# Kernel optimization log

Hardware: AMD Instinct MI355X
Metric: run time of the kernel (lower is better)

The kernel has to match this reference:

```python
import jax, jax.numpy as jnp
import numpy as np
from jax import lax

B, S, D, H, O = 128, 256, 128, 512, 25
TEMP = 0.1


def _init(key, shape, scale):
    return jax.random.uniform(key, shape, jnp.float32, -scale, scale)


def setup_inputs() -> dict:
    key = jax.random.key(0)
    ks = jax.random.split(key, 24)
    sH = 1.0 / np.sqrt(H)
    s2H = 1.0 / np.sqrt(2 * H)
    sD = 1.0 / np.sqrt(D)
    inp = {
        "x": jax.random.normal(ks[0], (B, S, D), jnp.float32),
        "noise_u": jnp.clip(jax.random.uniform(ks[1], (S, B, 1), jnp.float32), 1e-6, 1 - 1e-6),
        # layer_cin: Linear(D, H)
        "w_cin": _init(ks[2], (D, H), sD), "b_cin": _init(ks[3], (H,), sD),
        # layer_c MLP: 2H->2H (x3, ReLU) -> 1
        "w1": _init(ks[4], (2 * H, 2 * H), s2H), "b1": _init(ks[5], (2 * H,), s2H),
        "w2": _init(ks[6], (2 * H, 2 * H), s2H), "b2": _init(ks[7], (2 * H,), s2H),
        "w3": _init(ks[8], (2 * H, 2 * H), s2H), "b3": _init(ks[9], (2 * H,), s2H),
        "w4": _init(ks[10], (2 * H, 1), s2H), "b4": _init(ks[11], (1,), s2H),
        # GRUCell(H, H): gates ordered (r, z, n)
        "w_ih": _init(ks[12], (H, 3 * H), sH), "b_ih": _init(ks[13], (3 * H,), sH),
        "w_hh": _init(ks[14], (H, 3 * H), sH), "b_hh": _init(ks[15], (3 * H,), sH),
        # output Linear(H, O)
        "w_out": _init(ks[16], (H, O), sH), "b_out": _init(ks[17], (O,), sH),
    }
    return inp


def _gru_cell(x, h, w_ih, b_ih, w_hh, b_hh):
    gx = x @ w_ih + b_ih  # [B, 3H]
    gh = h @ w_hh + b_hh
    xr, xz, xn = jnp.split(gx, 3, axis=-1)
    hr, hz, hn = jnp.split(gh, 3, axis=-1)
    r = jax.nn.sigmoid(xr + hr)
    z = jax.nn.sigmoid(xz + hz)
    n = jnp.tanh(xn + r * hn)
    return (1.0 - z) * n + z * h


def reference(x, noise_u, w_cin, b_cin, w1, b1, w2, b2, w3, b3, w4, b4,
              w_ih, b_ih, w_hh, b_hh, w_out, b_out):
    xs = jnp.transpose(x, (1, 0, 2))  # [S, B, D]

    def step(carry, inp):
        c, h, n = carry
        x_t, u = inp
        c_in = jnp.tanh(x_t @ w_cin + b_cin)  # [B, H]
        com = jnp.concatenate([c, c_in], axis=1)  # [B, 2H]
        z = jax.nn.relu(com @ w1 + b1)
        z = jax.nn.relu(z @ w2 + b2)
        z = jax.nn.relu(z @ w3 + b3)
        alpha_logit = z @ w4 + b4  # [B, 1]
        # RelaxedBernoulli(temp=0.1).sample(): sigmoid((logits + logistic noise)/T), detached
        logistic = jnp.log(u) - jnp.log1p(-u)
        alpha = lax.stop_gradient(jax.nn.sigmoid((alpha_logit + logistic) / TEMP))
        h_gru = _gru_cell(c, h, w_ih, b_ih, w_hh, b_hh)
        h_new = h * (1.0 - alpha) + alpha * h_gru
        new_n = n * (1.0 - alpha) + 1.0
        c_new = (c * n * (1.0 - alpha) + c_in) / new_n
        return (c_new, h_new, new_n), None

    c0 = jnp.zeros((B, H), x.dtype)
    h0 = jnp.zeros((B, H), x.dtype)
    n0 = jnp.zeros((B, 1), x.dtype)
    (c, h, n), _ = lax.scan(step, (c0, h0, n0), (xs, noise_u))
    h = _gru_cell(c, h, w_ih, b_ih, w_hh, b_hh)  # final post-loop GRU step
    return h @ w_out + b_out
```

## Files before the change

### kernel.cpp

```cpp
#include <hip/hip_runtime.h>
#include <math.h>

#define SLEN 256
#define BSZ  128
#define DIN  128
#define HSZ  512
#define HH2  1024
#define GG3  1536
#define OSZ  25
#define SPIN_LIMIT (1 << 22)

typedef _Float16 h8 __attribute__((ext_vector_type(8)));
typedef _Float16 h4v __attribute__((ext_vector_type(4)));
typedef float    f4 __attribute__((ext_vector_type(4)));

struct P_t {
  const float *x, *noise, *b_cin, *b1, *b2, *b3, *w4, *b4, *b_ih, *b_hh, *w_out, *b_out;
  _Float16 *WT1, *WT2, *WT3, *WTih, *WThh, *WTcin;
  _Float16 *FW1T, *FW1B, *FW2, *FW3, *FWih, *FWhh;
  _Float16 *CIN, *Z1, *Z2, *HGRU16;
  float *LOGI, *C1, *D1, *CIH, *G;
  float *A1, *AIH, *AHH, *HF, *HGRUF, *NF, *PART;
  int *CNT;
  float *out;
};

__device__ __forceinline__ f4 mfma16(h8 a, h8 b, f4 c) {
  return __builtin_amdgcn_mfma_f32_16x16x32_f16(a, b, c, 0, 0, 0);
}

__global__ __launch_bounds__(256) void transpose_cvt(const float* __restrict__ src,
    _Float16* __restrict__ dst, int K, int N) {
  __shared__ float tl[32][33];
  int nt = N >> 5;
  int bx = blockIdx.x % nt, by = blockIdx.x / nt;
  int n0 = bx << 5, k0 = by << 5;
  int tx = threadIdx.x & 31, ty = threadIdx.x >> 5;
#pragma unroll
  for (int i = 0; i < 4; ++i) {
    int r = ty + (i << 3);
    tl[r][tx] = src[(size_t)(k0 + r) * N + n0 + tx];
  }
  __syncthreads();
#pragma unroll
  for (int i = 0; i < 4; ++i) {
    int r = ty + (i << 3);
    dst[(size_t)(n0 + r) * K + k0 + tx] = (_Float16)tl[tx][r];
  }
}

__global__ __launch_bounds__(512) void fragpack2(const _Float16* __restrict__ src,
    _Float16* __restrict__ dst, int srcK, int kOff, int K) {
  int ct = blockIdx.x;
  int chunks = (K / 32) * 64;
  for (int idx = threadIdx.x; idx < chunks; idx += 512) {
    int i = idx >> 6, lane = idx & 63;
    int mlw = lane & 15, qw = lane >> 4;
    *(h8*)(dst + ((size_t)ct * (K / 32) + i) * 512 + (size_t)lane * 8) =
        *(const h8*)(src + ((size_t)ct * 16 + mlw) * srcK + kOff + i * 32 + qw * 8);
  }
}

__global__ __launch_bounds__(256) void cin_kernel(P_t P) {
  int tid = blockIdx.x * blockDim.x + threadIdx.x;
  if (tid < SLEN * BSZ) {
    float u = P.noise[tid];
    P.LOGI[tid] = logf(u) - log1pf(-u);
  }
  int gw = tid >> 6, lane = tid & 63;
  int nw = (gridDim.x * blockDim.x) >> 6;
  int ml = lane & 15, q = lane >> 4;
  const int MT = (SLEN * BSZ) / 16;
  for (int tt = gw; tt < MT * 8; tt += nw) {
    int mt = tt & (MT - 1), nt = tt / MT;
    int m0 = mt * 16, n0 = nt * 64;
    int m = m0 + ml, b = m & 127, s = m >> 7;
    const float* ap = P.x + ((size_t)b * SLEN + s) * DIN + q * 8;
    const _Float16* bp = P.WTcin + (size_t)(n0 + ml) * DIN + q * 8;
    f4 a0 = {0,0,0,0}, a1 = a0, a2 = a0, a3 = a0;
#pragma unroll
    for (int k = 0; k < DIN; k += 32) {
      f4 lo = *(const f4*)(ap + k);
      f4 hi = *(const f4*)(ap + k + 4);
      h8 av;
      av[0] = (_Float16)lo[0]; av[1] = (_Float16)lo[1];
      av[2] = (_Float16)lo[2]; av[3] = (_Float16)lo[3];
      av[4] = (_Float16)hi[0]; av[5] = (_Float16)hi[1];
      av[6] = (_Float16)hi[2]; av[7] = (_Float16)hi[3];
      a0 = mfma16(av, *(const h8*)(bp + k),            a0);
      a1 = mfma16(av, *(const h8*)(bp + 16*DIN + k),   a1);
      a2 = mfma16(av, *(const h8*)(bp + 32*DIN + k),   a2);
      a3 = mfma16(av, *(const h8*)(bp + 48*DIN + k),   a3);
    }
#pragma unroll
    for (int r = 0; r < 4; ++r) {
      int row = m0 + q * 4 + r;
      int c0 = n0 + ml;
      P.CIN[(size_t)row * HSZ + c0     ] = (_Float16)tanhf(a0[r] + P.b_cin[c0]);
      P.CIN[(size_t)row * HSZ + c0 + 16] = (_Float16)tanhf(a1[r] + P.b_cin[c0 + 16]);
      P.CIN[(size_t)row * HSZ + c0 + 32] = (_Float16)tanhf(a2[r] + P.b_cin[c0 + 32]);
      P.CIN[(size_t)row * HSZ + c0 + 48] = (_Float16)tanhf(a3[r] + P.b_cin[c0 + 48]);
    }
  }
}

__global__ __launch_bounds__(256) void init_kernel(P_t P) {
  int idx = blockIdx.x * 256 + threadIdx.x;
  for (int i = idx; i < BSZ * GG3; i += 65536) { P.AIH[i] = 0.f; P.AHH[i] = 0.f; }
  for (int i = idx; i < BSZ * HH2; i += 65536) P.A1[i] = 0.f;
  if (idx < BSZ * HSZ) P.HF[idx] = 0.f;
  if (idx < 2 * BSZ) P.NF[idx] = 0.f;
  if (idx < 128) P.CNT[idx] = 0;
}

__global__ __launch_bounds__(256) void boot_kernel(P_t P) {
  const int tid = threadIdx.x, lane = tid & 63, wv = tid >> 6;
  const int ml = lane & 15, q = lane >> 4;
  const int g = blockIdx.x * 4 + wv;
  {
    int rt = g & 7, ct = g >> 3, m0 = rt << 4, col = (ct << 4) + ml;
    const _Float16* a0 = P.CIN + (size_t)(m0 + ml) * HSZ + q * 8;
    const _Float16* bp = P.FW1B + (size_t)ct * 16 * 512 + (size_t)lane * 8;
    f4 acc = {0.f, 0.f, 0.f, 0.f};
#pragma unroll
    for (int k = 0; k < 16; ++k)
      acc = mfma16(*(const h8*)(a0 + k * 32), *(const h8*)(bp + (size_t)k * 512), acc);
    float bia = P.b1[col];
#pragma unroll
    for (int j = 0; j < 4; ++j)
      P.Z1[(size_t)(m0 + q * 4 + j) * HH2 + col] = (_Float16)fmaxf(acc[j] + bia, 0.f);
  }
  int e = blockIdx.x * 512 + tid;
#pragma unroll
  for (int rep = 0; rep < 2; ++rep, e += 256) {
    int row = e >> 9, cc = e & 511;
    float rg = 1.f / (1.f + expf(-(P.b_ih[cc] + P.b_hh[cc])));
    float zg = 1.f / (1.f + expf(-(P.b_ih[cc + 512] + P.b_hh[cc + 512])));
    float ng = tanhf(P.b_ih[cc + 1024] + rg * P.b_hh[cc + 1024]);
    float v = (1.f - zg) * ng;
    P.HGRUF[(size_t)row * HSZ + cc] = v;
    P.HGRU16[(size_t)row * HSZ + cc] = (_Float16)v;
  }
}

__global__ __launch_bounds__(256) void node_a(P_t P, int t) {
  const int tid = threadIdx.x, lane = tid & 63, wv = tid >> 6;
  const int ml = lane & 15, q = lane >> 4;
  const int g = blockIdx.x * 4 + wv;
  f4 acc = {0.f, 0.f, 0.f, 0.f};
  if (g < 512) {
    int rt = g & 7, ct = g >> 3, m0 = rt << 4, col = (ct << 4) + ml;
    const _Float16* a0 = P.Z1 + (size_t)(m0 + ml) * HH2 + q * 8;
    const _Float16* bp = P.FW2 + (size_t)ct * 32 * 512 + (size_t)lane * 8;
#pragma unroll
    for (int k = 0; k < 32; ++k)
      acc = mfma16(*(const h8*)(a0 + k * 32), *(const h8*)(bp + (size_t)k * 512), acc);
    float bia = P.b2[col];
#pragma unroll
    for (int j = 0; j < 4; ++j)
      P.Z2[(size_t)(m0 + q * 4 + j) * HH2 + col] = (_Float16)fmaxf(acc[j] + bia, 0.f);
  } else if (g < 1280) {
    int u = g - 512, rt = u & 7, ct = u >> 3, m0 = rt << 4, col = (ct << 4) + ml;
    const _Float16* a0 = P.HGRU16 + (size_t)(m0 + ml) * HSZ + q * 8;
    const _Float16* bp = P.FWhh + (size_t)ct * 16 * 512 + (size_t)lane * 8;
#pragma unroll
    for (int k = 0; k < 16; ++k)
      acc = mfma16(*(const h8*)(a0 + k * 32), *(const h8*)(bp + (size_t)k * 512), acc);
#pragma unroll
    for (int j = 0; j < 4; ++j)
      P.G[(size_t)(m0 + q * 4 + j) * GG3 + col] = acc[j];
  } else if (g < 1792) {
    int u = g - 1280, rt = u & 7, ct = u >> 3, m0 = rt << 4, col = (ct << 4) + ml;
    const _Float16* a0 = P.CIN + ((size_t)t * BSZ + m0 + ml) * HSZ + q * 8;
    const _Float16* bp = P.FW1T + (size_t)ct * 16 * 512 + (size_t)lane * 8;
#pragma unroll
    for (int k = 0; k < 16; ++k)
      acc = mfma16(*(const h8*)(a0 + k * 32), *(const h8*)(bp + (size_t)k * 512), acc);
#pragma unroll
    for (int j = 0; j < 4; ++j)
      P.C1[(size_t)(m0 + q * 4 + j) * HH2 + col] = acc[j];
  } else if (g < 2560) {
    int u = g - 1792, rt = u & 7, ct = u >> 3, m0 = rt << 4, col = (ct << 4) + ml;
    const _Float16* a0 = P.CIN + ((size_t)t * BSZ + m0 + ml) * HSZ + q * 8;
    const _Float16* bp = P.FWih + (size_t)ct * 16 * 512 + (size_t)lane * 8;
#pragma unroll
    for (int k = 0; k < 16; ++k)
      acc = mfma16(*(const h8*)(a0 + k * 32), *(const h8*)(bp + (size_t)k * 512), acc);
#pragma unroll
    for (int j = 0; j < 4; ++j)
      P.CIH[(size_t)(m0 + q * 4 + j) * GG3 + col] = acc[j];
  } else {
    if (t + 1 < SLEN) {
      int u = g - 2560, rt = u & 7, ct = u >> 3, m0 = rt << 4, col = (ct << 4) + ml;
      const _Float16* a0 = P.CIN + ((size_t)(t + 1) * BSZ + m0 + ml) * HSZ + q * 8;
      const _Float16* bp = P.FW1B + (size_t)ct * 16 * 512 + (size_t)lane * 8;
#pragma unroll
      for (int k = 0; k < 16; ++k)
        acc = mfma16(*(const h8*)(a0 + k * 32), *(const h8*)(bp + (size_t)k * 512), acc);
#pragma unroll
      for (int j = 0; j < 4; ++j)
        P.D1[(size_t)(m0 + q * 4 + j) * HH2 + col] = acc[j];
    }
  }
}

__global__ __launch_bounds__(256) void node_b(P_t P, int t) {
  const int tid = threadIdx.x, lane = tid & 63, wv = tid >> 6;
  const int ml = lane & 15, q = lane >> 4;
  const int b = blockIdx.x, rt = b & 7, sub = b >> 3;
  const int m0 = rt << 4;
  __shared__ float sAl[16], sNN[16];

  {
    int ct = sub * 4 + wv, col = (ct << 4) + ml;
    const _Float16* a0 = P.Z2 + (size_t)(m0 + ml) * HH2 + q * 8;
    const _Float16* bp = P.FW3 + (size_t)ct * 32 * 512 + (size_t)lane * 8;
    f4 acc = {0.f, 0.f, 0.f, 0.f};
#pragma unroll
    for (int k = 0; k < 32; ++k)
      acc = mfma16(*(const h8*)(a0 + k * 32), *(const h8*)(bp + (size_t)k * 512), acc);
    float bia = P.b3[col], w4v = P.w4[col];
#pragma unroll
    for (int j = 0; j < 4; ++j) {
      float v = fmaxf(acc[j] + bia, 0.f) * w4v;
      v += __shfl_xor(v, 1); v += __shfl_xor(v, 2);
      v += __shfl_xor(v, 4); v += __shfl_xor(v, 8);
      if (ml == 0)
        __hip_atomic_store(&P.PART[(size_t)ct * BSZ + m0 + q * 4 + j], v,
                           __ATOMIC_RELAXED, __HIP_MEMORY_SCOPE_AGENT);
    }
  }
  asm volatile("s_waitcnt vmcnt(0)" ::: "memory");
  __syncthreads();
  if (tid == 0) {
    __hip_atomic_fetch_add(&P.CNT[rt * 16], 1, __ATOMIC_RELAXED, __HIP_MEMORY_SCOPE_AGENT);
    const int target = 16 * (t + 1);
    int tries = 0;
    while (__hip_atomic_load(&P.CNT[rt * 16], __ATOMIC_RELAXED,
                             __HIP_MEMORY_SCOPE_AGENT) < target) {
      if (++tries > SPIN_LIMIT) break;
      __builtin_amdgcn_s_sleep(1);
    }
  }
  __syncthreads();

  {
    int rl = tid >> 4, sg = tid & 15, row = m0 + rl;
    float v = 0.f;
#pragma unroll
    for (int k2 = 0; k2 < 4; ++k2)
      v += __hip_atomic_load(&P.PART[(size_t)(sg * 4 + k2) * BSZ + row],
                             __ATOMIC_RELAXED, __HIP_MEMORY_SCOPE_AGENT);
    v += __shfl_xor(v, 1); v += __shfl_xor(v, 2);
    v += __shfl_xor(v, 4); v += __shfl_xor(v, 8);
    if (sg == 0) {
      float lg = (v + P.b4[0] + P.LOGI[(size_t)t * BSZ + row]) * 10.0f;
      float al = 1.f / (1.f + expf(-lg));
      float no = P.NF[((t + 1) & 1) * BSZ + row];
      float nn = no * (1.f - al) + 1.f;
      sAl[rl] = al; sNN[rl] = nn;
      if (sub == 0) P.NF[(t & 1) * BSZ + row] = nn;
    }
  }
  __syncthreads();

  {
    int rl = tid >> 4, row = m0 + rl;
    int c0 = sub * 64 + (tid & 15) * 4;
    float al = sAl[rl], om = 1.f - al, rin = 1.f / sNN[rl];
    size_t o = (size_t)row * HH2 + c0;
    f4 a = *(f4*)(P.A1 + o);
    f4 c1 = *(const f4*)(P.C1 + o);
#pragma unroll
    for (int j = 0; j < 4; ++j) a[j] = om * a[j] + c1[j];
    *(f4*)(P.A1 + o) = a;
    if (t + 1 < SLEN) {
      f4 d = *(const f4*)(P.D1 + o);
      f4 bb = *(const f4*)(P.b1 + c0);
      h4v zo;
#pragma unroll
      for (int j = 0; j < 4; ++j)
        zo[j] = (_Float16)fmaxf(a[j] * rin + d[j] + bb[j], 0.f);
      *(h4v*)(P.Z1 + o) = zo;
    }
  }

  {
    int rl = tid >> 4, row = m0 + rl;
    float al = sAl[rl], om = 1.f - al, rin = 1.f / sNN[rl];
    int cbase = sub * 32 + (tid & 15) * 2;
#pragma unroll
    for (int e = 0; e < 2; ++e) {
      int cc = cbase + e;
      size_t o3 = (size_t)row * GG3 + cc;
      float air = om * P.AIH[o3]        + P.CIH[o3];
      float aiz = om * P.AIH[o3 + 512]  + P.CIH[o3 + 512];
      float ain = om * P.AIH[o3 + 1024] + P.CIH[o3 + 1024];
      P.AIH[o3] = air; P.AIH[o3 + 512] = aiz; P.AIH[o3 + 1024] = ain;
      float ahr = om * P.AHH[o3]        + al * P.G[o3];
      float ahz = om * P.AHH[o3 + 512]  + al * P.G[o3 + 512];
      float ahn = om * P.AHH[o3 + 1024] + al * P.G[o3 + 1024];
      P.AHH[o3] = ahr; P.AHH[o3 + 512] = ahz; P.AHH[o3 + 1024] = ahn;
      float gxr = air * rin + P.b_ih[cc];
      float gxz = aiz * rin + P.b_ih[cc + 512];
      float gxn = ain * rin + P.b_ih[cc + 1024];
      float ghr = ahr + P.b_hh[cc];
      float ghz = ahz + P.b_hh[cc + 512];
      float ghn = ahn + P.b_hh[cc + 1024];
      float rg = 1.f / (1.f + expf(-(gxr + ghr)));
      float zg = 1.f / (1.f + expf(-(gxz + ghz)));
      float ng = tanhf(gxn + rg * ghn);
      size_t oh = (size_t)row * HSZ + cc;
      float hold = P.HF[oh];
      float hgt  = P.HGRUF[oh];
      float hnew = om * hold + al * hgt;
      P.HF[oh] = hnew;
      float hg1 = (1.f - zg) * ng + zg * hnew;
      P.HGRUF[oh] = hg1;
      P.HGRU16[oh] = (_Float16)hg1;
    }
  }
}

__global__ __launch_bounds__(256) void final_out(P_t P) {
  __shared__ float hf[512];
  const int r = blockIdx.x, tid = threadIdx.x;
  const int lane = tid & 63, wv = tid >> 6;
  for (int e = tid; e < 512; e += 256) hf[e] = P.HGRUF[(size_t)r * HSZ + e];
  __syncthreads();
  for (int c = wv; c < OSZ; c += 4) {
    float v = 0.f;
#pragma unroll
    for (int j = 0; j < 8; ++j)
      v += hf[lane + 64 * j] * P.w_out[(size_t)(lane + 64 * j) * OSZ + c];
    for (int off = 32; off > 0; off >>= 1) v += __shfl_xor(v, off);
    if (lane == 0) P.out[r * OSZ + c] = v + P.b_out[c];
  }
}

extern "C" void kernel_launch(void* const* d_in, const int* in_sizes, int n_in,
                              void* d_out, int out_size, void* d_ws, size_t ws_size,
                              hipStream_t stream) {
  const float* x     = (const float*)d_in[0];
  const float* noise = (const float*)d_in[1];
  const float* w_cin = (const float*)d_in[2];
  const float* b_cin = (const float*)d_in[3];
  const float* w1    = (const float*)d_in[4];
  const float* b1    = (const float*)d_in[5];
  const float* w2    = (const float*)d_in[6];
  const float* b2    = (const float*)d_in[7];
  const float* w3    = (const float*)d_in[8];
  const float* b3    = (const float*)d_in[9];
  const float* w4    = (const float*)d_in[10];
  const float* b4    = (const float*)d_in[11];
  const float* w_ih  = (const float*)d_in[12];
  const float* b_ih  = (const float*)d_in[13];
  const float* w_hh  = (const float*)d_in[14];
  const float* b_hh  = (const float*)d_in[15];
  const float* w_out = (const float*)d_in[16];
  const float* b_out = (const float*)d_in[17];

  char* ws = (char*)d_ws;
  size_t off = 0;
  auto alloc = [&](size_t bytes) -> void* {
    void* p = ws + off;
    off = (off + bytes + 255) & ~(size_t)255;
    return p;
  };

  P_t P;
  P.x = x; P.noise = noise; P.b_cin = b_cin; P.b1 = b1; P.b2 = b2; P.b3 = b3;
  P.w4 = w4; P.b4 = b4; P.b_ih = b_ih; P.b_hh = b_hh; P.w_out = w_out; P.b_out = b_out;
  P.WT1    = (_Float16*)alloc((size_t)HH2 * HH2 * 2);
  P.WT2    = (_Float16*)alloc((size_t)HH2 * HH2 * 2);
  P.WT3    = (_Float16*)alloc((size_t)HH2 * HH2 * 2);
  P.WTih   = (_Float16*)alloc((size_t)GG3 * HSZ * 2);
  P.WThh   = (_Float16*)alloc((size_t)GG3 * HSZ * 2);
  P.WTcin  = (_Float16*)alloc((size_t)HSZ * DIN * 2);
  P.FW1T   = (_Float16*)alloc((size_t)HH2 * 512 * 2);
  P.FW1B   = (_Float16*)alloc((size_t)HH2 * 512 * 2);
  P.FW2    = (_Float16*)alloc((size_t)HH2 * HH2 * 2);
  P.FW3    = (_Float16*)alloc((size_t)HH2 * HH2 * 2);
  P.FWih   = (_Float16*)alloc((size_t)GG3 * HSZ * 2);
  P.FWhh   = (_Float16*)alloc((size_t)GG3 * HSZ * 2);
  P.CIN    = (_Float16*)alloc((size_t)SLEN * BSZ * HSZ * 2);
  P.Z1     = (_Float16*)alloc((size_t)BSZ * HH2 * 2);
  P.Z2     = (_Float16*)alloc((size_t)BSZ * HH2 * 2);
  P.HGRU16 = (_Float16*)alloc((size_t)BSZ * HSZ * 2);
  P.LOGI   = (float*)alloc((size_t)SLEN * BSZ * 4);
  P.C1     = (float*)alloc((size_t)BSZ * HH2 * 4);
  P.D1     = (float*)alloc((size_t)BSZ * HH2 * 4);
  P.CIH    = (float*)alloc((size_t)BSZ * GG3 * 4);
  P.G      = (float*)alloc((size_t)BSZ * GG3 * 4);
  P.A1     = (float*)alloc((size_t)BSZ * HH2 * 4);
  P.AIH    = (float*)alloc((size_t)BSZ * GG3 * 4);
  P.AHH    = (float*)alloc((size_t)BSZ * GG3 * 4);
  P.HF     = (float*)alloc((size_t)BSZ * HSZ * 4);
  P.HGRUF  = (float*)alloc((size_t)BSZ * HSZ * 4);
  P.NF     = (float*)alloc((size_t)2 * BSZ * 4);
  P.PART   = (float*)alloc((size_t)64 * BSZ * 4);
  P.CNT    = (int*)alloc(128 * 4);
  P.out    = (float*)d_out;

  transpose_cvt<<<(HH2/32)*(HH2/32), 256, 0, stream>>>(w1, P.WT1, HH2, HH2);
  transpose_cvt<<<(HH2/32)*(HH2/32), 256, 0, stream>>>(w2, P.WT2, HH2, HH2);
  transpose_cvt<<<(HH2/32)*(HH2/32), 256, 0, stream>>>(w3, P.WT3, HH2, HH2);
  transpose_cvt<<<(GG3/32)*(HSZ/32), 256, 0, stream>>>(w_ih, P.WTih, HSZ, GG3);
  transpose_cvt<<<(GG3/32)*(HSZ/32), 256, 0, stream>>>(w_hh, P.WThh, HSZ, GG3);
  transpose_cvt<<<(HSZ/32)*(DIN/32), 256, 0, stream>>>(w_cin, P.WTcin, DIN, HSZ);
  fragpack2<<<HH2/16, 512, 0, stream>>>(P.WT1, P.FW1T, HH2, 0, 512);
  fragpack2<<<HH2/16, 512, 0, stream>>>(P.WT1, P.FW1B, HH2, 512, 512);
  fragpack2<<<HH2/16, 512, 0, stream>>>(P.WT2, P.FW2, HH2, 0, HH2);
  fragpack2<<<HH2/16, 512, 0, stream>>>(P.WT3, P.FW3, HH2, 0, HH2);
  fragpack2<<<GG3/16, 512, 0, stream>>>(P.WTih, P.FWih, HSZ, 0, HSZ);
  fragpack2<<<GG3/16, 512, 0, stream>>>(P.WThh, P.FWhh, HSZ, 0, HSZ);

  cin_kernel<<<1024, 256, 0, stream>>>(P);
  init_kernel<<<256, 256, 0, stream>>>(P);
  boot_kernel<<<128, 256, 0, stream>>>(P);

  for (int t = 0; t < SLEN; ++t) {
    node_a<<<768, 256, 0, stream>>>(P, t);
    node_b<<<128, 256, 0, stream>>>(P, t);
  }
  final_out<<<BSZ, 256, 0, stream>>>(P);
}
```

Baseline: 6.443 ms.

## Fuse per-step node kernels into one launch with row-tile spin barriers

Merges node_a and node_b into a single step_node kernel of 256 blocks × 512 threads. Each step now uses one launch instead of two, with two in-kernel counter barriers per 16-row tile replacing the kernel boundary. GRU gate buffers are interleaved per column (r,z,n) so the elementwise update reads contiguous triples, and Z2 is staged through LDS for the W3 GEMM. This removes a launch per timestep and the global round-trip between the kernels. In exchange it adds spin-wait costs and depends on all 256 blocks being co-resident, with a timeout fallback that could yield wrong results if blocks are not all scheduled.

```diff
diff --git a/kernel.cpp b/kernel.cpp
--- a/kernel.cpp
+++ b/kernel.cpp
@@ -8,7 +8,6 @@
 #define HH2  1024
 #define GG3  1536
 #define OSZ  25
-#define SPIN_LIMIT (1 << 22)
 
 typedef _Float16 h8 __attribute__((ext_vector_type(8)));
 typedef _Float16 h4v __attribute__((ext_vector_type(4)));
@@ -19,14 +18,47 @@
   _Float16 *WT1, *WT2, *WT3, *WTih, *WThh, *WTcin;
   _Float16 *FW1T, *FW1B, *FW2, *FW3, *FWih, *FWhh;
   _Float16 *CIN, *Z1, *Z2, *HGRU16;
-  float *LOGI, *C1, *D1, *CIH, *G;
-  float *A1, *AIH, *AHH, *HF, *HGRUF, *NF, *PART;
-  int *CNT;
+  float *LOGI, *C1, *D1, *CIH3, *G3;
+  float *A1, *AIH3, *AHH3, *HF, *HGRUF, *NF, *PART;
+  int *CNT, *DEAD;
   float *out;
 };
 
 __device__ __forceinline__ f4 mfma16(h8 a, h8 b, f4 c) {
   return __builtin_amdgcn_mfma_f32_16x16x32_f16(a, b, c, 0, 0, 0);
+}
+
+__device__ __forceinline__ float ldc_f(const float* p) {
+  return __hip_atomic_load(p, __ATOMIC_RELAXED, __HIP_MEMORY_SCOPE_AGENT);
+}
+__device__ __forceinline__ void stc_f(float* p, float v) {
+  __hip_atomic_store(p, v, __ATOMIC_RELAXED, __HIP_MEMORY_SCOPE_AGENT);
+}
+__device__ __forceinline__ unsigned ldc_u(const unsigned* p) {
+  return __hip_atomic_load(p, __ATOMIC_RELAXED, __HIP_MEMORY_SCOPE_AGENT);
+}
+__device__ __forceinline__ void stc_u(unsigned* p, unsigned v) {
+  __hip_atomic_store(p, v, __ATOMIC_RELAXED, __HIP_MEMORY_SCOPE_AGENT);
+}
+
+__device__ __forceinline__ void rtbar(int* cnt, int target, int* dead) {
+  asm volatile("s_waitcnt vmcnt(0)" ::: "memory");
+  __syncthreads();
+  if (threadIdx.x == 0) {
+    __hip_atomic_fetch_add(cnt, 1, __ATOMIC_RELAXED, __HIP_MEMORY_SCOPE_AGENT);
+    int tries = 0;
+    while (__hip_atomic_load(cnt, __ATOMIC_RELAXED, __HIP_MEMORY_SCOPE_AGENT) < target) {
+      if (((++tries) & 63) == 0) {
+        if (tries > (1 << 16) ||
+            __hip_atomic_load(dead, __ATOMIC_RELAXED, __HIP_MEMORY_SCOPE_AGENT)) {
+          __hip_atomic_store(dead, 1, __ATOMIC_RELAXED, __HIP_MEMORY_SCOPE_AGENT);
+          break;
+        }
+      }
+      __builtin_amdgcn_s_sleep(2);
+    }
+  }
+  __syncthreads();
 }
 
 __global__ __launch_bounds__(256) void transpose_cvt(const float* __restrict__ src,
@@ -106,11 +138,12 @@
 
 __global__ __launch_bounds__(256) void init_kernel(P_t P) {
   int idx = blockIdx.x * 256 + threadIdx.x;
-  for (int i = idx; i < BSZ * GG3; i += 65536) { P.AIH[i] = 0.f; P.AHH[i] = 0.f; }
   for (int i = idx; i < BSZ * HH2; i += 65536) P.A1[i] = 0.f;
+  for (int i = idx; i < BSZ * HSZ * 3; i += 65536) { P.AIH3[i] = 0.f; P.AHH3[i] = 0.f; }
   if (idx < BSZ * HSZ) P.HF[idx] = 0.f;
   if (idx < 2 * BSZ) P.NF[idx] = 0.f;
   if (idx < 128) P.CNT[idx] = 0;
+  if (idx == 0) P.DEAD[0] = 0;
 }
 
 __global__ __launch_bounds__(256) void boot_kernel(P_t P) {
@@ -143,77 +176,119 @@
   }
 }
 
-__global__ __launch_bounds__(256) void node_a(P_t P, int t) {
-  const int tid = threadIdx.x, lane = tid & 63, wv = tid >> 6;
+__global__ __launch_bounds__(512, 2) void step_node(P_t P, int t) {
+  const int tid = threadIdx.x;
+  const int lane = tid & 63, wv = tid >> 6;
   const int ml = lane & 15, q = lane >> 4;
-  const int g = blockIdx.x * 4 + wv;
-  f4 acc = {0.f, 0.f, 0.f, 0.f};
-  if (g < 512) {
-    int rt = g & 7, ct = g >> 3, m0 = rt << 4, col = (ct << 4) + ml;
+  const int b = blockIdx.x, rt = b >> 5, sub = b & 31;
+  const int m0 = rt << 4;
+  const int slot = sub * 8 + wv;
+  __shared__ unsigned sZd[16 * 516];
+  __shared__ float sAl[16], sNN[16];
+  int* cnt  = P.CNT + rt * 16;
+  int* dead = P.DEAD;
+
+  if (sub < 8) {
+    int ct = slot, col = (ct << 4) + ml;
     const _Float16* a0 = P.Z1 + (size_t)(m0 + ml) * HH2 + q * 8;
     const _Float16* bp = P.FW2 + (size_t)ct * 32 * 512 + (size_t)lane * 8;
+    f4 acc = {0.f, 0.f, 0.f, 0.f};
 #pragma unroll
     for (int k = 0; k < 32; ++k)
       acc = mfma16(*(const h8*)(a0 + k * 32), *(const h8*)(bp + (size_t)k * 512), acc);
     float bia = P.b2[col];
 #pragma unroll
-    for (int j = 0; j < 4; ++j)
-      P.Z2[(size_t)(m0 + q * 4 + j) * HH2 + col] = (_Float16)fmaxf(acc[j] + bia, 0.f);
-  } else if (g < 1280) {
-    int u = g - 512, rt = u & 7, ct = u >> 3, m0 = rt << 4, col = (ct << 4) + ml;
-    const _Float16* a0 = P.HGRU16 + (size_t)(m0 + ml) * HSZ + q * 8;
-    const _Float16* bp = P.FWhh + (size_t)ct * 16 * 512 + (size_t)lane * 8;
-#pragma unroll
-    for (int k = 0; k < 16; ++k)
-      acc = mfma16(*(const h8*)(a0 + k * 32), *(const h8*)(bp + (size_t)k * 512), acc);
-#pragma unroll
-    for (int j = 0; j < 4; ++j)
-      P.G[(size_t)(m0 + q * 4 + j) * GG3 + col] = acc[j];
-  } else if (g < 1792) {
-    int u = g - 1280, rt = u & 7, ct = u >> 3, m0 = rt << 4, col = (ct << 4) + ml;
-    const _Float16* a0 = P.CIN + ((size_t)t * BSZ + m0 + ml) * HSZ + q * 8;
-    const _Float16* bp = P.FW1T + (size_t)ct * 16 * 512 + (size_t)lane * 8;
-#pragma unroll
-    for (int k = 0; k < 16; ++k)
-      acc = mfma16(*(const h8*)(a0 + k * 32), *(const h8*)(bp + (size_t)k * 512), acc);
-#pragma unroll
-    for (int j = 0; j < 4; ++j)
-      P.C1[(size_t)(m0 + q * 4 + j) * HH2 + col] = acc[j];
-  } else if (g < 2560) {
-    int u = g - 1792, rt = u & 7, ct = u >> 3, m0 = rt << 4, col = (ct << 4) + ml;
-    const _Float16* a0 = P.CIN + ((size_t)t * BSZ + m0 + ml) * HSZ + q * 8;
-    const _Float16* bp = P.FWih + (size_t)ct * 16 * 512 + (size_t)lane * 8;
-#pragma unroll
-    for (int k = 0; k < 16; ++k)
-      acc = mfma16(*(const h8*)(a0 + k * 32), *(const h8*)(bp + (size_t)k * 512), acc);
-#pragma unroll
-    for (int j = 0; j < 4; ++j)
-      P.CIH[(size_t)(m0 + q * 4 + j) * GG3 + col] = acc[j];
+    for (int j = 0; j < 4; ++j) {
+      _Float16 hv = (_Float16)fmaxf(acc[j] + bia, 0.f);
+      unsigned short mb = __builtin_bit_cast(unsigned short, hv);
+      unsigned ob = (unsigned)__shfl_xor((int)mb, 1) & 0xffffu;
+      if (!(ml & 1))
+        stc_u((unsigned*)&P.Z2[(size_t)(m0 + q * 4 + j) * HH2 + col],
+              (unsigned)mb | (ob << 16));
+    }
   } else {
-    if (t + 1 < SLEN) {
-      int u = g - 2560, rt = u & 7, ct = u >> 3, m0 = rt << 4, col = (ct << 4) + ml;
-      const _Float16* a0 = P.CIN + ((size_t)(t + 1) * BSZ + m0 + ml) * HSZ + q * 8;
-      const _Float16* bp = P.FW1B + (size_t)ct * 16 * 512 + (size_t)lane * 8;
-#pragma unroll
-      for (int k = 0; k < 16; ++k)
-        acc = mfma16(*(const h8*)(a0 + k * 32), *(const h8*)(bp + (size_t)k * 512), acc);
-#pragma unroll
-      for (int j = 0; j < 4; ++j)
-        P.D1[(size_t)(m0 + q * 4 + j) * HH2 + col] = acc[j];
-    }
-  }
-}
-
-__global__ __launch_bounds__(256) void node_b(P_t P, int t) {
-  const int tid = threadIdx.x, lane = tid & 63, wv = tid >> 6;
-  const int ml = lane & 15, q = lane >> 4;
-  const int b = blockIdx.x, rt = b & 7, sub = b >> 3;
-  const int m0 = rt << 4;
-  __shared__ float sAl[16], sNN[16];
-
-  {
-    int ct = sub * 4 + wv, col = (ct << 4) + ml;
-    const _Float16* a0 = P.Z2 + (size_t)(m0 + ml) * HH2 + q * 8;
+    int ts = slot - 64;
+    for (int e = ts; e < 320; e += 192) {
+      f4 acc = {0.f, 0.f, 0.f, 0.f};
+      if (e < 96) {
+        int ct = e, col = (ct << 4) + ml;
+        const _Float16* a0 = P.HGRU16 + (size_t)(m0 + ml) * HSZ + q * 8;
+        const _Float16* bp = P.FWhh + (size_t)ct * 16 * 512 + (size_t)lane * 8;
+#pragma unroll
+        for (int k = 0; k < 16; ++k)
+          acc = mfma16(*(const h8*)(a0 + k * 32), *(const h8*)(bp + (size_t)k * 512), acc);
+        int gate = col >> 9, cc = col & 511;
+#pragma unroll
+        for (int j = 0; j < 4; ++j)
+          stc_f(P.G3 + ((size_t)(m0 + q * 4 + j) * 512 + cc) * 3 + gate, acc[j]);
+      } else if (e < 160) {
+        int ct = e - 96, col = (ct << 4) + ml;
+        const _Float16* a0 = P.CIN + ((size_t)t * BSZ + m0 + ml) * HSZ + q * 8;
+        const _Float16* bp = P.FW1T + (size_t)ct * 16 * 512 + (size_t)lane * 8;
+#pragma unroll
+        for (int k = 0; k < 16; ++k)
+          acc = mfma16(*(const h8*)(a0 + k * 32), *(const h8*)(bp + (size_t)k * 512), acc);
+#pragma unroll
+        for (int j = 0; j < 4; ++j)
+          stc_f(P.C1 + (size_t)(m0 + q * 4 + j) * HH2 + col, acc[j]);
+      } else if (e < 256) {
+        int ct = e - 160, col = (ct << 4) + ml;
+        const _Float16* a0 = P.CIN + ((size_t)t * BSZ + m0 + ml) * HSZ + q * 8;
+        const _Float16* bp = P.FWih + (size_t)ct * 16 * 512 + (size_t)lane * 8;
+#pragma unroll
+        for (int k = 0; k < 16; ++k)
+          acc = mfma16(*(const h8*)(a0 + k * 32), *(const h8*)(bp + (size_t)k * 512), acc);
+        int gate = col >> 9, cc = col & 511;
+#pragma unroll
+        for (int j = 0; j < 4; ++j)
+          stc_f(P.CIH3 + ((size_t)(m0 + q * 4 + j) * 512 + cc) * 3 + gate, acc[j]);
+      } else if (t + 1 < SLEN) {
+        int ct = e - 256, col = (ct << 4) + ml;
+        const _Float16* a0 = P.CIN + ((size_t)(t + 1) * BSZ + m0 + ml) * HSZ + q * 8;
+        const _Float16* bp = P.FW1B + (size_t)ct * 16 * 512 + (size_t)lane * 8;
+#pragma unroll
+        for (int k = 0; k < 16; ++k)
+          acc = mfma16(*(const h8*)(a0 + k * 32), *(const h8*)(bp + (size_t)k * 512), acc);
+#pragma unroll
+        for (int j = 0; j < 4; ++j)
+          stc_f(P.D1 + (size_t)(m0 + q * 4 + j) * HH2 + col, acc[j]);
+      }
+    }
+  }
+  rtbar(cnt, t * 64 + 32, dead);
+
+  const int rA = tid >> 5, cA = (sub << 5) + (tid & 31);
+  const size_t oA = (size_t)(m0 + rA) * HH2 + cA;
+  float c1v = ldc_f(P.C1 + oA);
+  float d1v = (t + 1 < SLEN) ? ldc_f(P.D1 + oA) : 0.f;
+  float a1old = P.A1[oA];
+  float b1v = P.b1[cA];
+  const int r3 = tid >> 4, cc3 = (sub << 4) + (tid & 15);
+  const size_t o3 = ((size_t)(m0 + r3) * 512 + cc3) * 3;
+  const size_t oh = (size_t)(m0 + r3) * HSZ + cc3;
+  float cih0 = 0, cih1 = 0, cih2 = 0, g0 = 0, g1 = 0, g2 = 0;
+  float aih0 = 0, aih1 = 0, aih2 = 0, ahh0 = 0, ahh1 = 0, ahh2 = 0;
+  float bi0 = 0, bi1 = 0, bi2 = 0, bh0 = 0, bh1 = 0, bh2 = 0;
+  float hfold = 0, hgrold = 0;
+  if (tid < 256) {
+    cih0 = ldc_f(P.CIH3 + o3); cih1 = ldc_f(P.CIH3 + o3 + 1); cih2 = ldc_f(P.CIH3 + o3 + 2);
+    g0 = ldc_f(P.G3 + o3); g1 = ldc_f(P.G3 + o3 + 1); g2 = ldc_f(P.G3 + o3 + 2);
+    aih0 = P.AIH3[o3]; aih1 = P.AIH3[o3 + 1]; aih2 = P.AIH3[o3 + 2];
+    ahh0 = P.AHH3[o3]; ahh1 = P.AHH3[o3 + 1]; ahh2 = P.AHH3[o3 + 2];
+    bi0 = P.b_ih[cc3]; bi1 = P.b_ih[cc3 + 512]; bi2 = P.b_ih[cc3 + 1024];
+    bh0 = P.b_hh[cc3]; bh1 = P.b_hh[cc3 + 512]; bh2 = P.b_hh[cc3 + 1024];
+    hfold = P.HF[oh]; hgrold = P.HGRUF[oh];
+  }
+  if (sub < 8) {
+    unsigned vb[16];
+    const unsigned* z2d = (const unsigned*)P.Z2 + (size_t)m0 * 512;
+#pragma unroll
+    for (int j = 0; j < 16; ++j) vb[j] = ldc_u(z2d + (size_t)j * 512 + tid);
+#pragma unroll
+    for (int j = 0; j < 16; ++j) sZd[j * 516 + tid] = vb[j];
+    __syncthreads();
+    int ct = slot, col = (ct << 4) + ml;
+    const _Float16* a0 = (const _Float16*)sZd + ml * 1032 + q * 8;
     const _Float16* bp = P.FW3 + (size_t)ct * 32 * 512 + (size_t)lane * 8;
     f4 acc = {0.f, 0.f, 0.f, 0.f};
 #pragma unroll
@@ -225,100 +300,52 @@
       float v = fmaxf(acc[j] + bia, 0.f) * w4v;
       v += __shfl_xor(v, 1); v += __shfl_xor(v, 2);
       v += __shfl_xor(v, 4); v += __shfl_xor(v, 8);
-      if (ml == 0)
-        __hip_atomic_store(&P.PART[(size_t)ct * BSZ + m0 + q * 4 + j], v,
-                           __ATOMIC_RELAXED, __HIP_MEMORY_SCOPE_AGENT);
-    }
-  }
-  asm volatile("s_waitcnt vmcnt(0)" ::: "memory");
-  __syncthreads();
-  if (tid == 0) {
-    __hip_atomic_fetch_add(&P.CNT[rt * 16], 1, __ATOMIC_RELAXED, __HIP_MEMORY_SCOPE_AGENT);
-    const int target = 16 * (t + 1);
-    int tries = 0;
-    while (__hip_atomic_load(&P.CNT[rt * 16], __ATOMIC_RELAXED,
-                             __HIP_MEMORY_SCOPE_AGENT) < target) {
-      if (++tries > SPIN_LIMIT) break;
-      __builtin_amdgcn_s_sleep(1);
-    }
-  }
-  __syncthreads();
-
-  {
-    int rl = tid >> 4, sg = tid & 15, row = m0 + rl;
+      if (ml == 0) stc_f(P.PART + (size_t)ct * BSZ + m0 + q * 4 + j, v);
+    }
+  }
+  rtbar(cnt, t * 64 + 64, dead);
+
+  if (wv == 0) {
+    int r = lane & 15, pq = lane >> 4;
+    int row = m0 + r;
     float v = 0.f;
 #pragma unroll
-    for (int k2 = 0; k2 < 4; ++k2)
-      v += __hip_atomic_load(&P.PART[(size_t)(sg * 4 + k2) * BSZ + row],
-                             __ATOMIC_RELAXED, __HIP_MEMORY_SCOPE_AGENT);
-    v += __shfl_xor(v, 1); v += __shfl_xor(v, 2);
-    v += __shfl_xor(v, 4); v += __shfl_xor(v, 8);
-    if (sg == 0) {
+    for (int k = 0; k < 16; ++k)
+      v += ldc_f(P.PART + (size_t)(pq * 16 + k) * BSZ + row);
+    v += __shfl_xor(v, 16); v += __shfl_xor(v, 32);
+    if (lane < 16) {
       float lg = (v + P.b4[0] + P.LOGI[(size_t)t * BSZ + row]) * 10.0f;
       float al = 1.f / (1.f + expf(-lg));
       float no = P.NF[((t + 1) & 1) * BSZ + row];
       float nn = no * (1.f - al) + 1.f;
-      sAl[rl] = al; sNN[rl] = nn;
+      sAl[r] = al; sNN[r] = nn;
       if (sub == 0) P.NF[(t & 1) * BSZ + row] = nn;
     }
   }
   __syncthreads();
-
   {
-    int rl = tid >> 4, row = m0 + rl;
-    int c0 = sub * 64 + (tid & 15) * 4;
-    float al = sAl[rl], om = 1.f - al, rin = 1.f / sNN[rl];
-    size_t o = (size_t)row * HH2 + c0;
-    f4 a = *(f4*)(P.A1 + o);
-    f4 c1 = *(const f4*)(P.C1 + o);
-#pragma unroll
-    for (int j = 0; j < 4; ++j) a[j] = om * a[j] + c1[j];
-    *(f4*)(P.A1 + o) = a;
-    if (t + 1 < SLEN) {
-      f4 d = *(const f4*)(P.D1 + o);
-      f4 bb = *(const f4*)(P.b1 + c0);
-      h4v zo;
-#pragma unroll
-      for (int j = 0; j < 4; ++j)
-        zo[j] = (_Float16)fmaxf(a[j] * rin + d[j] + bb[j], 0.f);
-      *(h4v*)(P.Z1 + o) = zo;
-    }
-  }
-
-  {
-    int rl = tid >> 4, row = m0 + rl;
-    float al = sAl[rl], om = 1.f - al, rin = 1.f / sNN[rl];
-    int cbase = sub * 32 + (tid & 15) * 2;
-#pragma unroll
-    for (int e = 0; e < 2; ++e) {
-      int cc = cbase + e;
-      size_t o3 = (size_t)row * GG3 + cc;
-      float air = om * P.AIH[o3]        + P.CIH[o3];
-      float aiz = om * P.AIH[o3 + 512]  + P.CIH[o3 + 512];
-      float ain = om * P.AIH[o3 + 1024] + P.CIH[o3 + 1024];
-      P.AIH[o3] = air; P.AIH[o3 + 512] = aiz; P.AIH[o3 + 1024] = ain;
-      float ahr = om * P.AHH[o3]        + al * P.G[o3];
-      float ahz = om * P.AHH[o3 + 512]  + al * P.G[o3 + 512];
-      float ahn = om * P.AHH[o3 + 1024] + al * P.G[o3 + 1024];
-      P.AHH[o3] = ahr; P.AHH[o3 + 512] = ahz; P.AHH[o3 + 1024] = ahn;
-      float gxr = air * rin + P.b_ih[cc];
-      float gxz = aiz * rin + P.b_ih[cc + 512];
-      float gxn = ain * rin + P.b_ih[cc + 1024];
-      float ghr = ahr + P.b_hh[cc];
-      float ghz = ahz + P.b_hh[cc + 512];
-      float ghn = ahn + P.b_hh[cc + 1024];
-      float rg = 1.f / (1.f + expf(-(gxr + ghr)));
-      float zg = 1.f / (1.f + expf(-(gxz + ghz)));
-      float ng = tanhf(gxn + rg * ghn);
-      size_t oh = (size_t)row * HSZ + cc;
-      float hold = P.HF[oh];
-      float hgt  = P.HGRUF[oh];
-      float hnew = om * hold + al * hgt;
-      P.HF[oh] = hnew;
-      float hg1 = (1.f - zg) * ng + zg * hnew;
-      P.HGRUF[oh] = hg1;
-      P.HGRU16[oh] = (_Float16)hg1;
-    }
+    float al = sAl[rA], om = 1.f - al, rin = 1.f / sNN[rA];
+    float a = om * a1old + c1v;
+    P.A1[oA] = a;
+    if (t + 1 < SLEN)
+      P.Z1[oA] = (_Float16)fmaxf(a * rin + d1v + b1v, 0.f);
+  }
+  if (tid < 256) {
+    float al = sAl[r3], om = 1.f - al, rin = 1.f / sNN[r3];
+    float air = om * aih0 + cih0, aiz = om * aih1 + cih1, ain = om * aih2 + cih2;
+    P.AIH3[o3] = air; P.AIH3[o3 + 1] = aiz; P.AIH3[o3 + 2] = ain;
+    float ahr = om * ahh0 + al * g0, ahz = om * ahh1 + al * g1, ahn = om * ahh2 + al * g2;
+    P.AHH3[o3] = ahr; P.AHH3[o3 + 1] = ahz; P.AHH3[o3 + 2] = ahn;
+    float gxr = air * rin + bi0, gxz = aiz * rin + bi1, gxn = ain * rin + bi2;
+    float ghr = ahr + bh0, ghz = ahz + bh1, ghn = ahn + bh2;
+    float rg = 1.f / (1.f + expf(-(gxr + ghr)));
+    float zg = 1.f / (1.f + expf(-(gxz + ghz)));
+    float ng = tanhf(gxn + rg * ghn);
+    float hnew = om * hfold + al * hgrold;
+    P.HF[oh] = hnew;
+    float hg1 = (1.f - zg) * ng + zg * hnew;
+    P.HGRUF[oh] = hg1;
+    P.HGRU16[oh] = (_Float16)hg1;
   }
 }
 
@@ -390,16 +417,17 @@
   P.LOGI   = (float*)alloc((size_t)SLEN * BSZ * 4);
   P.C1     = (float*)alloc((size_t)BSZ * HH2 * 4);
   P.D1     = (float*)alloc((size_t)BSZ * HH2 * 4);
-  P.CIH    = (float*)alloc((size_t)BSZ * GG3 * 4);
-  P.G      = (float*)alloc((size_t)BSZ * GG3 * 4);
+  P.CIH3   = (float*)alloc((size_t)BSZ * HSZ * 3 * 4);
+  P.G3     = (float*)alloc((size_t)BSZ * HSZ * 3 * 4);
   P.A1     = (float*)alloc((size_t)BSZ * HH2 * 4);
-  P.AIH    = (float*)alloc((size_t)BSZ * GG3 * 4);
-  P.AHH    = (float*)alloc((size_t)BSZ * GG3 * 4);
+  P.AIH3   = (float*)alloc((size_t)BSZ * HSZ * 3 * 4);
+  P.AHH3   = (float*)alloc((size_t)BSZ * HSZ * 3 * 4);
   P.HF     = (float*)alloc((size_t)BSZ * HSZ * 4);
   P.HGRUF  = (float*)alloc((size_t)BSZ * HSZ * 4);
   P.NF     = (float*)alloc((size_t)2 * BSZ * 4);
   P.PART   = (float*)alloc((size_t)64 * BSZ * 4);
   P.CNT    = (int*)alloc(128 * 4);
+  P.DEAD   = (int*)alloc(64 * 4);
   P.out    = (float*)d_out;
 
   transpose_cvt<<<(HH2/32)*(HH2/32), 256, 0, stream>>>(w1, P.WT1, HH2, HH2);
@@ -419,9 +447,7 @@
   init_kernel<<<256, 256, 0, stream>>>(P);
   boot_kernel<<<128, 256, 0, stream>>>(P);
 
-  for (int t = 0; t < SLEN; ++t) {
-    node_a<<<768, 256, 0, stream>>>(P, t);
-    node_b<<<128, 256, 0, stream>>>(P, t);
-  }
+  for (int t = 0; t < SLEN; ++t)
+    step_node<<<256, 512, 0, stream>>>(P, t);
   final_out<<<BSZ, 256, 0, stream>>>(P);
 }
```

Measured after the change: 7.281 ms. 13.0% more time.
